# Optimization experiments

Hardware: AMD Instinct MI355X
Metric: run time of the kernel (lower is better)

The kernel has to match this reference:

```python
import jax, jax.numpy as jnp
import numpy as np

K = 3  # kernel size, padding=1, stride=1, dilation=1 (torchvision deform_conv2d defaults used)


def _bilinear_sample(img, y, x):
    """Bilinear sample img (B,H,W) at float coords y,x (B,T,H,W) with zero padding
    outside the image, matching torchvision's deform_conv2d bilinear rule
    (each of the four corner taps is zeroed individually when out of range)."""
    B, H, W = img.shape
    y0f = jnp.floor(y)
    x0f = jnp.floor(x)
    ly = y - y0f  # fractional parts
    lx = x - x0f
    hy = 1.0 - ly
    hx = 1.0 - lx
    y0 = y0f.astype(jnp.int32)
    x0 = x0f.astype(jnp.int32)
    y1 = y0 + 1
    x1 = x0 + 1

    img_flat = img.reshape(B, H * W)

    def corner(yi, xi):
        valid = ((yi >= 0) & (yi < H) & (xi >= 0) & (xi < W)).astype(img.dtype)
        yc = jnp.clip(yi, 0, H - 1)
        xc = jnp.clip(xi, 0, W - 1)
        flat = (yc * W + xc).reshape(B, -1)  # (B, T*H*W)
        g = jax.vmap(lambda im, f: im[f])(img_flat, flat).reshape(yi.shape)
        return g * valid

    v00 = corner(y0, x0)
    v01 = corner(y0, x1)
    v10 = corner(y1, x0)
    v11 = corner(y1, x1)
    return hy * hx * v00 + hy * lx * v01 + ly * hx * v10 + ly * lx * v11


def deform_conv2d_1ch(inp, weight, offset):
    # inp: (B,H,W); weight: (1,1,3,3); offset: (B, 2*K*K, H, W)
    B, H, W = inp.shape
    off = offset.reshape(B, K * K, 2, H, W)
    oy = off[:, :, 0]  # (B,9,H,W) y-offsets
    ox = off[:, :, 1]  # (B,9,H,W) x-offsets
    kh, kw = jnp.meshgrid(jnp.arange(K), jnp.arange(K), indexing='ij')
    ky = (kh.reshape(-1) - 1).astype(inp.dtype)  # pad=1 -> tap offsets in {-1,0,1}
    kx = (kw.reshape(-1) - 1).astype(inp.dtype)
    hh = jnp.arange(H, dtype=inp.dtype)
    ww = jnp.arange(W, dtype=inp.dtype)
    y = hh[None, None, :, None] + ky[None, :, None, None] + oy  # (B,9,H,W)
    x = ww[None, None, None, :] + kx[None, :, None, None] + ox
    sampled = _bilinear_sample(inp, y, x)  # (B,9,H,W)
    wk = weight.reshape(K * K)
    return jnp.einsum('k,bkhw->bhw', wk, sampled)


def setup_inputs() -> dict:
    key = jax.random.key(0)
    k1, k2, k3 = jax.random.split(key, 3)
    B, H, W = 8, 512, 512
    inp = jax.random.normal(k1, (B, H, W), dtype=jnp.float32)
    weight = jax.random.uniform(k2, (1, 1, K, K), dtype=jnp.float32)
    offset = jax.random.uniform(k3, (B, 2 * K * K, H, W), dtype=jnp.float32)
    return {"input": inp, "weight": weight, "offset": offset}


def reference(input, weight, offset):
    return deform_conv2d_1ch(input, weight, offset)
```

## Files before the change

### kernel.cpp

```cpp
#include <hip/hip_runtime.h>

constexpr int K  = 3;
constexpr int Hc = 512, Wc = 512, Bc = 8;
constexpr int HWc = Hc * Wc;

#if __has_builtin(__builtin_amdgcn_make_buffer_rsrc) && __has_builtin(__builtin_amdgcn_raw_buffer_load_b32)
#define USE_BUF 1
#else
#define USE_BUF 0
#endif

__global__ __launch_bounds__(256, 6) void deform_conv2d_kernel(
    const float* __restrict__ inp,
    const float* __restrict__ wgt,
    const float* __restrict__ off,
    float* __restrict__ out)
{
    const int p  = blockIdx.x * blockDim.x + threadIdx.x;
    const int b  = p >> 18;
    const int hw = p & (HWc - 1);
    const int h  = hw >> 9;
    const int w  = hw & (Wc - 1);

    const float* __restrict__ img  = inp + (size_t)b * HWc;
    const float* __restrict__ offb = off + (size_t)b * (2 * K * K) * HWc + hw;

    float oy[K * K], ox[K * K];
#pragma unroll
    for (int k = 0; k < K * K; ++k) {
        oy[k] = offb[(2 * k)     * HWc];
        ox[k] = offb[(2 * k + 1) * HWc];
    }

#if USE_BUF
    __amdgpu_buffer_rsrc_t rsrc = __builtin_amdgcn_make_buffer_rsrc(
        (void*)img, (short)0, HWc * 4, 0x00020000);
#endif

    float acc = 0.f;

#pragma unroll
    for (int k = 0; k < K * K; ++k) {
        const int ky = k / K - 1;
        const int kx = k % K - 1;

        const float y = (float)(h + ky) + oy[k];
        const float x = (float)(w + kx) + ox[k];

        const float y0f = floorf(y);
        const float x0f = floorf(x);
        const float ly = y - y0f, lx = x - x0f;
        const int y0 = (int)y0f, x0 = (int)x0f;

        float v00, v01, v10, v11;

#if USE_BUF
        const int fb = (y0 << 9) + x0;
        const int fbB = fb * 4;
        v00 = __uint_as_float(__builtin_amdgcn_raw_buffer_load_b32(rsrc, fbB,            0, 0));
        v01 = __uint_as_float(__builtin_amdgcn_raw_buffer_load_b32(rsrc, fbB + 4,        0, 0));
        v10 = __uint_as_float(__builtin_amdgcn_raw_buffer_load_b32(rsrc, fbB + Wc*4,     0, 0));
        v11 = __uint_as_float(__builtin_amdgcn_raw_buffer_load_b32(rsrc, fbB + Wc*4 + 4, 0, 0));
        const bool vx0 = (unsigned)x0       < (unsigned)Wc;
        const bool vx1 = (unsigned)(x0 + 1) < (unsigned)Wc;
        v00 = vx0 ? v00 : 0.f;   v10 = vx0 ? v10 : 0.f;
        v01 = vx1 ? v01 : 0.f;   v11 = vx1 ? v11 : 0.f;
#else
        const int y1 = y0 + 1, x1 = x0 + 1;
        auto corner = [&](int yi, int xi) -> float {
            const bool valid = ((unsigned)yi < (unsigned)Hc) & ((unsigned)xi < (unsigned)Wc);
            return valid ? img[yi * Wc + xi] : 0.f;
        };
        v00 = corner(y0, x0); v01 = corner(y0, x1);
        v10 = corner(y1, x0); v11 = corner(y1, x1);
#endif

        const float top = v00 + lx * (v01 - v00);
        const float bot = v10 + lx * (v11 - v10);
        acc += wgt[k] * (top + ly * (bot - top));
    }

    out[p] = acc;
}

extern "C" void kernel_launch(void* const* d_in, const int* in_sizes, int n_in,
                              void* d_out, int out_size, void* d_ws, size_t ws_size,
                              hipStream_t stream)
{
    const float* inp = (const float*)d_in[0];
    const float* wgt = (const float*)d_in[1];
    const float* off = (const float*)d_in[2];
    float* out = (float*)d_out;

    const int npix  = Bc * HWc;
    const int block = 256;
    const int grid  = npix / block;

    deform_conv2d_kernel<<<grid, block, 0, stream>>>(inp, wgt, off, out);
}
```

Before: 39.95 us.

## Add shared 4x4 neighbourhood fast path when all offsets lie in [0,1)

Computes the min and max of the 18 offsets per pixel. When every lane in the wavefront has offsets in [0,1), all nine taps fall inside a fixed 4x4 window, so the kernel loads 16 values instead of 36 and reuses them across adjacent taps. Otherwise it falls back to the generic per-tap gather. Offset loads also move to buffer loads, and the launch bound rises to 8 waves per SIMD. The fast path's x-bounds handling relies on buffer out-of-range returning zero for rows off the image, and its use is driven by the uniform [0,1) offsets in the test inputs.

```diff
diff --git a/kernel.cpp b/kernel.cpp
--- a/kernel.cpp
+++ b/kernel.cpp
@@ -4,13 +4,32 @@
 constexpr int Hc = 512, Wc = 512, Bc = 8;
 constexpr int HWc = Hc * Wc;
 
-#if __has_builtin(__builtin_amdgcn_make_buffer_rsrc) && __has_builtin(__builtin_amdgcn_raw_buffer_load_b32)
-#define USE_BUF 1
-#else
-#define USE_BUF 0
-#endif
+__device__ __forceinline__ float bload(__amdgpu_buffer_rsrc_t r, int vo, int so) {
+    return __uint_as_float(__builtin_amdgcn_raw_buffer_load_b32(r, vo, so, 0));
+}
 
-__global__ __launch_bounds__(256, 6) void deform_conv2d_kernel(
+#define LOADROW(V0, V1, V2, V3, RB)                                  \
+    V0 = bload(irsrc, fbB + (RB),      0);                           \
+    V1 = bload(irsrc, fbB + (RB) + 4,  0);                           \
+    V2 = bload(irsrc, fbB + (RB) + 8,  0);                           \
+    V3 = bload(irsrc, fbB + (RB) + 12, 0);                           \
+    V0 = c0 ? V0 : 0.f; V2 = c2 ? V2 : 0.f; V3 = c3 ? V3 : 0.f;
+
+#define TAPROW(A0, A1, A2, A3, B0, B1, B2, B3, KB)                   \
+    {                                                                \
+        float t, bo;                                                 \
+        t  = A0 + ox[KB]     * (A1 - A0);                            \
+        bo = B0 + ox[KB]     * (B1 - B0);                            \
+        acc += wk[KB]     * (t + oy[KB]     * (bo - t));             \
+        t  = A1 + ox[KB + 1] * (A2 - A1);                            \
+        bo = B1 + ox[KB + 1] * (B2 - B1);                            \
+        acc += wk[KB + 1] * (t + oy[KB + 1] * (bo - t));             \
+        t  = A2 + ox[KB + 2] * (A3 - A2);                            \
+        bo = B2 + ox[KB + 2] * (B3 - B2);                            \
+        acc += wk[KB + 2] * (t + oy[KB + 2] * (bo - t));             \
+    }
+
+__global__ __launch_bounds__(256, 8) void deform_conv2d_kernel(
     const float* __restrict__ inp,
     const float* __restrict__ wgt,
     const float* __restrict__ off,
@@ -22,62 +41,77 @@
     const int h  = hw >> 9;
     const int w  = hw & (Wc - 1);
 
-    const float* __restrict__ img  = inp + (size_t)b * HWc;
-    const float* __restrict__ offb = off + (size_t)b * (2 * K * K) * HWc + hw;
+    __amdgpu_buffer_rsrc_t orsrc = __builtin_amdgcn_make_buffer_rsrc(
+        (void*)(off + (size_t)b * (2 * K * K) * HWc), (short)0,
+        (2 * K * K) * HWc * 4, 0x00020000);
+    __amdgpu_buffer_rsrc_t irsrc = __builtin_amdgcn_make_buffer_rsrc(
+        (void*)(inp + (size_t)b * HWc), (short)0, HWc * 4, 0x00020000);
+
+    const int hwB = hw * 4;
 
     float oy[K * K], ox[K * K];
 #pragma unroll
     for (int k = 0; k < K * K; ++k) {
-        oy[k] = offb[(2 * k)     * HWc];
-        ox[k] = offb[(2 * k + 1) * HWc];
+        oy[k] = bload(orsrc, hwB, (2 * k)     * HWc * 4);
+        ox[k] = bload(orsrc, hwB, (2 * k + 1) * HWc * 4);
     }
 
-#if USE_BUF
-    __amdgpu_buffer_rsrc_t rsrc = __builtin_amdgcn_make_buffer_rsrc(
-        (void*)img, (short)0, HWc * 4, 0x00020000);
-#endif
+    float mn = fminf(oy[0], ox[0]);
+    float mx = fmaxf(oy[0], ox[0]);
+#pragma unroll
+    for (int k = 1; k < K * K; ++k) {
+        mn = fminf(mn, fminf(oy[k], ox[k]));
+        mx = fmaxf(mx, fmaxf(oy[k], ox[k]));
+    }
+
+    float wk[K * K];
+#pragma unroll
+    for (int k = 0; k < K * K; ++k) wk[k] = wgt[k];
 
     float acc = 0.f;
 
+    if (__all((mn >= 0.f) & (mx < 1.f))) {
+        const int  fbB = ((h - 1) * Wc + (w - 1)) * 4;
+        const bool c0 = (w >= 1);
+        const bool c2 = (w <= Wc - 2);
+        const bool c3 = (w <= Wc - 3);
+
+        float a0, a1, a2, a3, b0, b1, b2, b3;
+        LOADROW(a0, a1, a2, a3, 0)
+        LOADROW(b0, b1, b2, b3, Wc * 4)
+        TAPROW(a0, a1, a2, a3, b0, b1, b2, b3, 0)
+        LOADROW(a0, a1, a2, a3, 2 * Wc * 4)
+        TAPROW(b0, b1, b2, b3, a0, a1, a2, a3, 3)
+        LOADROW(b0, b1, b2, b3, 3 * Wc * 4)
+        TAPROW(a0, a1, a2, a3, b0, b1, b2, b3, 6)
+    } else {
 #pragma unroll
-    for (int k = 0; k < K * K; ++k) {
-        const int ky = k / K - 1;
-        const int kx = k % K - 1;
+        for (int k = 0; k < K * K; ++k) {
+            const int ky = k / K - 1;
+            const int kx = k % K - 1;
 
-        const float y = (float)(h + ky) + oy[k];
-        const float x = (float)(w + kx) + ox[k];
+            const float y = (float)(h + ky) + oy[k];
+            const float x = (float)(w + kx) + ox[k];
 
-        const float y0f = floorf(y);
-        const float x0f = floorf(x);
-        const float ly = y - y0f, lx = x - x0f;
-        const int y0 = (int)y0f, x0 = (int)x0f;
+            const float y0f = floorf(y);
+            const float x0f = floorf(x);
+            const float ly = y - y0f, lx = x - x0f;
+            const int y0 = (int)y0f, x0 = (int)x0f;
 
-        float v00, v01, v10, v11;
+            const int fbB = ((y0 << 9) + x0) * 4;
+            float v00 = bload(irsrc, fbB,              0);
+            float v01 = bload(irsrc, fbB + 4,          0);
+            float v10 = bload(irsrc, fbB + Wc * 4,     0);
+            float v11 = bload(irsrc, fbB + Wc * 4 + 4, 0);
+            const bool vx0 = (unsigned)x0       < (unsigned)Wc;
+            const bool vx1 = (unsigned)(x0 + 1) < (unsigned)Wc;
+            v00 = vx0 ? v00 : 0.f;   v10 = vx0 ? v10 : 0.f;
+            v01 = vx1 ? v01 : 0.f;   v11 = vx1 ? v11 : 0.f;
 
-#if USE_BUF
-        const int fb = (y0 << 9) + x0;
-        const int fbB = fb * 4;
-        v00 = __uint_as_float(__builtin_amdgcn_raw_buffer_load_b32(rsrc, fbB,            0, 0));
-        v01 = __uint_as_float(__builtin_amdgcn_raw_buffer_load_b32(rsrc, fbB + 4,        0, 0));
-        v10 = __uint_as_float(__builtin_amdgcn_raw_buffer_load_b32(rsrc, fbB + Wc*4,     0, 0));
-        v11 = __uint_as_float(__builtin_amdgcn_raw_buffer_load_b32(rsrc, fbB + Wc*4 + 4, 0, 0));
-        const bool vx0 = (unsigned)x0       < (unsigned)Wc;
-        const bool vx1 = (unsigned)(x0 + 1) < (unsigned)Wc;
-        v00 = vx0 ? v00 : 0.f;   v10 = vx0 ? v10 : 0.f;
-        v01 = vx1 ? v01 : 0.f;   v11 = vx1 ? v11 : 0.f;
-#else
-        const int y1 = y0 + 1, x1 = x0 + 1;
-        auto corner = [&](int yi, int xi) -> float {
-            const bool valid = ((unsigned)yi < (unsigned)Hc) & ((unsigned)xi < (unsigned)Wc);
-            return valid ? img[yi * Wc + xi] : 0.f;
-        };
-        v00 = corner(y0, x0); v01 = corner(y0, x1);
-        v10 = corner(y1, x0); v11 = corner(y1, x1);
-#endif
-
-        const float top = v00 + lx * (v01 - v00);
-        const float bot = v10 + lx * (v11 - v10);
-        acc += wgt[k] * (top + ly * (bot - top));
+            const float top = v00 + lx * (v01 - v00);
+            const float bot = v10 + lx * (v11 - v10);
+            acc += wk[k] * (top + ly * (bot - top));
+        }
     }
 
     out[p] = acc;
```

New measurement: 35.85 us. 1.11x faster.
